# Performance work log

Measured on AMD Instinct MI355X. Metric: run time of the kernel, lower is better.

The kernel has to match this reference:

```python
import jax, jax.numpy as jnp
import numpy as np

C = 32
C_Z = 128
S = 256
N_SEQ = 256
LN_EPS = 1e-5


def setup_inputs() -> dict:
    key = jax.random.key(0)
    k1, k2, k3, k4 = jax.random.split(key, 4)
    m_si = jax.random.normal(k1, (S, N_SEQ, C), dtype=jnp.float32)
    ln_gamma = jnp.ones((C,), dtype=jnp.float32)
    ln_beta = jnp.zeros((C,), dtype=jnp.float32)
    # nn.Linear(c, 2c, bias=False): weight shape (2c, c)
    W_ab = jax.random.normal(k2, (2 * C, C), dtype=jnp.float32) / np.sqrt(C)
    # nn.Linear(c*c, c_z): weight (c_z, c*c), bias (c_z,)
    W_out = jax.random.normal(k3, (C_Z, C * C), dtype=jnp.float32) / np.sqrt(C * C)
    b_out = jax.random.normal(k4, (C_Z,), dtype=jnp.float32) * 0.01
    return {"m_si": m_si, "ln_gamma": ln_gamma, "ln_beta": ln_beta,
            "W_ab": W_ab, "W_out": W_out, "b_out": b_out}


def reference(m_si, ln_gamma, ln_beta, W_ab, W_out, b_out):
    # LayerNorm over channel dim c
    mu = jnp.mean(m_si, axis=-1, keepdims=True)
    var = jnp.var(m_si, axis=-1, keepdims=True)
    x = (m_si - mu) * jax.lax.rsqrt(var + LN_EPS) * ln_gamma + ln_beta
    # linear_no_bias then chunk into a, b: each (s, n_seq, c)
    ab = jnp.einsum('snc,dc->snd', x, W_ab)
    a, b = ab[..., :C], ab[..., C:]
    # mean over MSA sequences of outer products a[s,i,:] x b[s,j,:]
    # restructured as a contraction over n_seq: (i, j, c, c)
    outer = jnp.einsum('inc,jnd->ijcd', a, b) / N_SEQ
    outer = outer.reshape(S, S, C * C)  # flatten (c, c) -> c*c
    # final linear projection to c_z
    z_ij = jnp.einsum('ijk,zk->ijz', outer, W_out) + b_out
    return z_ij
```

## Files before the change

### kernel.cpp

```cpp
#include <hip/hip_runtime.h>

#define SDIM 256
#define NSEQ 256
#define CDIM 32
#define CZ 128
#define IB 8
#define JB 4

typedef __bf16 bfx8 __attribute__((ext_vector_type(8)));
typedef float fx4 __attribute__((ext_vector_type(4)));
typedef float f32x16 __attribute__((ext_vector_type(16)));
typedef unsigned int u32x4 __attribute__((ext_vector_type(4)));

__device__ __forceinline__ unsigned short f2bf(float f) {
  unsigned int u = __float_as_uint(f);
  u += 0x7fffu + ((u >> 16) & 1u);
  return (unsigned short)(u >> 16);
}

__device__ __forceinline__ unsigned int cvtpk(float lo, float hi) {
  unsigned int r;
  asm("v_cvt_pk_bf16_f32 %0, %1, %2" : "=v"(r) : "v"(lo), "v"(hi));
  return r;
}

__device__ __forceinline__ void gload16(const void* g, void* l) {
  __builtin_amdgcn_global_load_lds((const __attribute__((address_space(1))) unsigned int*)g,
                                   (__attribute__((address_space(3))) unsigned int*)l,
                                   16, 0, 0);
}


__global__ __launch_bounds__(256) void opm_prep(
    const float* __restrict__ m_si, const float* __restrict__ gamma, const float* __restrict__ beta,
    const float* __restrict__ Wab, const float* __restrict__ Wout,
    unsigned short* __restrict__ a_t, unsigned short* __restrict__ b_t,
    unsigned short* __restrict__ w2T)
{
  const int b = blockIdx.x;
  const int t = threadIdx.x;
  if (b < 2 * SDIM) {
    const int s = b >> 1, dph = b & 1;
    __shared__ float wab[1024];
    __shared__ float gbuf[64];
    __shared__ __align__(16) char xbuf[36864];
    float* xin = (float*)xbuf;
    unsigned short* xt = (unsigned short*)xbuf;

    const float* msrc = m_si + s * 8192;
#pragma unroll
    for (int k = 0; k < 8; ++k) {
      const int q = t + k * 256;
      const int row = q >> 3, cq = q & 7;
      ((fx4*)xin)[row * 9 + cq] = ((const fx4*)msrc)[q];
    }
    for (int k = t; k < 1024; k += 256) wab[k] = Wab[dph * 1024 + k];
    if (t < 32) { gbuf[t] = gamma[t]; gbuf[32 + t] = beta[t]; }
    __syncthreads();

    float x[CDIM];
#pragma unroll
    for (int c = 0; c < CDIM; ++c) x[c] = xin[t * 36 + c];
    __syncthreads();

    float mu = 0.f;
#pragma unroll
    for (int c = 0; c < CDIM; ++c) mu += x[c];
    mu *= (1.f / CDIM);
    float var = 0.f;
#pragma unroll
    for (int c = 0; c < CDIM; ++c) { float d = x[c] - mu; var += d * d; }
    var *= (1.f / CDIM);
    const float inv = rsqrtf(var + 1e-5f);
#pragma unroll
    for (int c = 0; c < CDIM; ++c) x[c] = (x[c] - mu) * inv * gbuf[c] + gbuf[32 + c];

    for (int dp = 0; dp < 32; ++dp) {
      float sum = 0.f;
#pragma unroll
      for (int c = 0; c < CDIM; ++c) sum += x[c] * wab[dp * 32 + c];
      xt[dp * 256 + t] = f2bf(sum);
    }
    __syncthreads();

    unsigned short* outb = dph ? b_t : a_t;
#pragma unroll
    for (int k = 0; k < 4; ++k) {
      const int q = t + k * 256;
      const int row = q >> 5, cc = q & 31;
      *(u32x4*)(outb + (s * 32 + row) * 256 + cc * 8) = *(const u32x4*)(xbuf + row * 512 + cc * 16);
    }
  } else {
    const int base = ((b - 2 * SDIM) * 256 + t) * 64;
#pragma unroll 8
    for (int u = 0; u < 64; ++u) {
      const int dest = base + u;
      const int e  = dest & 7;
      const int zl = (dest >> 3) & 31;
      const int h  = (dest >> 8) & 1;
      const int ks = (dest >> 9) & 63;
      const int zt = dest >> 15;
      const int kp = ks * 16 + h * 8 + e;
      const int c = (kp & 3) | (((kp >> 8) & 1) << 2) | (((kp >> 2) & 1) << 3) | (((kp >> 9) & 1) << 4);
      const int d = (kp >> 3) & 31;
      const int z = zt * 32 + zl;
      w2T[dest] = f2bf(Wout[z * 1024 + c * CDIM + d]);
    }
  }
}

__global__ __launch_bounds__(512, 4) void opm_main(
    const unsigned short* __restrict__ a_t, const unsigned short* __restrict__ b_t,
    const unsigned short* __restrict__ w2T, const float* __restrict__ bout,
    float* __restrict__ out)
{
  __shared__ __align__(16) char smem[65536];
  char* o_sh = smem;

  const int tid = threadIdx.x;
  const int lane = tid & 63;
  const int wid = tid >> 6;
  const int l31 = lane & 31;
  const int h = lane >> 5;

  const int bxr = blockIdx.x;
  const int bx = (bxr & 7) * 256 + (bxr >> 3);
  const int i0 = (bx >> 6) * IB;
  const int j0 = (bx & 63) * JB;

  const int wm = wid >> 1;
  const int wn = wid & 1;
  const int wbase = wid * 1024;

  f32x16 acc00 = {}, acc01 = {}, acc10 = {}, acc11 = {};

  auto STAGE = [&](int buf, int nc) {
    const int nbase = nc * 32;
    char* A = smem + 16384 + buf * 16384;
    char* B = smem + 49152 + buf * 8192;
#pragma unroll
    for (int pass = 0; pass < 2; ++pass) {
      const int q = pass * 512 + tid;
      const int row = q >> 2;
      const int gs = (q & 3) ^ ((q >> 3) & 3);
      const unsigned short* src = a_t + ((i0 + (row >> 5)) * 32 + (row & 31)) * 256 + nbase + gs * 8;
      gload16(src, A + pass * 8192 + wbase);
    }
    {
      const int q = tid;
      const int row = q >> 2;
      const int gs = (q & 3) ^ ((q >> 3) & 3);
      const unsigned short* src = b_t + ((j0 + (row >> 5)) * 32 + (row & 31)) * 256 + nbase + gs * 8;
      gload16(src, B + wbase);
    }
  };

  auto COMPUTE = [&](int buf) {
    char* A = smem + 16384 + buf * 16384;
    char* B = smem + 49152 + buf * 8192;
#pragma unroll
    for (int ks = 0; ks < 2; ++ks) {
      const int s = ks * 2 + h;
      bfx8 af0, af1, bf0, bf1;
      { const int r = wm * 64 + l31;      af0 = *(const bfx8*)(A + r * 64 + (((s ^ (r >> 1)) & 3) << 4)); }
      { const int r = wm * 64 + 32 + l31; af1 = *(const bfx8*)(A + r * 64 + (((s ^ (r >> 1)) & 3) << 4)); }
      { const int r = wn * 64 + l31;      bf0 = *(const bfx8*)(B + r * 64 + (((s ^ (r >> 1)) & 3) << 4)); }
      { const int r = wn * 64 + 32 + l31; bf1 = *(const bfx8*)(B + r * 64 + (((s ^ (r >> 1)) & 3) << 4)); }
      __builtin_amdgcn_s_setprio(1);
      acc00 = __builtin_amdgcn_mfma_f32_32x32x16_bf16(af0, bf0, acc00, 0, 0, 0);
      acc01 = __builtin_amdgcn_mfma_f32_32x32x16_bf16(af0, bf1, acc01, 0, 0, 0);
      acc10 = __builtin_amdgcn_mfma_f32_32x32x16_bf16(af1, bf0, acc10, 0, 0, 0);
      acc11 = __builtin_amdgcn_mfma_f32_32x32x16_bf16(af1, bf1, acc11, 0, 0, 0);
      __builtin_amdgcn_s_setprio(0);
    }
  };

  STAGE(0, 0);
#pragma unroll 2
  for (int t = 0; t < 8; ++t) {
    if (t < 7) {
      STAGE((t + 1) & 1, t + 1);
      asm volatile("s_waitcnt vmcnt(3)" ::: "memory");
    } else {
      asm volatile("s_waitcnt vmcnt(0)" ::: "memory");
    }
    __builtin_amdgcn_s_barrier();
    asm volatile("" ::: "memory");
    COMPUTE(t & 1);
    asm volatile("s_waitcnt lgkmcnt(0)" ::: "memory");
    __builtin_amdgcn_s_barrier();
  }

  {
    const f32x16 av[4] = { acc00 * 0.00390625f, acc01 * 0.00390625f,
                           acc10 * 0.00390625f, acc11 * 0.00390625f };
#pragma unroll
    for (int mi = 0; mi < 2; ++mi) {
#pragma unroll
      for (int ni = 0; ni < 2; ++ni) {
        const f32x16 a = av[mi * 2 + ni];
        const int p = (wm * 2 + mi) * 4 + (wn * 2 + ni);
#pragma unroll
        for (int c4 = 0; c4 < 2; ++c4) {
          const int sl = l31 + 32 * h + 64 * c4;
          u32x4 v;
          v[0] = cvtpk(a[8 * c4 + 0], a[8 * c4 + 1]);
          v[1] = cvtpk(a[8 * c4 + 2], a[8 * c4 + 3]);
          v[2] = cvtpk(a[8 * c4 + 4], a[8 * c4 + 5]);
          v[3] = cvtpk(a[8 * c4 + 6], a[8 * c4 + 7]);
          *(u32x4*)(o_sh + p * 2048 + ((sl ^ (p & 7)) << 4)) = v;
        }
      }
    }
  }
  __syncthreads();

  {
    const int zt = wid & 3;
    const int kh = wid >> 2;
    const unsigned short* wp = w2T + (zt << 15) + (h << 8) + (l31 << 3);
    f32x16 accB = {};
    int ksg = kh * 32;
    bfx8 wfA = *(const bfx8*)(wp + (ksg << 9));
    bfx8 ofA = *(const bfx8*)(o_sh + l31 * 2048 + (((2 * ksg + h) ^ (l31 & 7)) << 4));
#pragma unroll
    for (int it = 0; it < 31; ++it) {
      const int kn = kh * 32 + it + 1;
      const bfx8 wfB = *(const bfx8*)(wp + (kn << 9));
      const bfx8 ofB = *(const bfx8*)(o_sh + l31 * 2048 + (((2 * kn + h) ^ (l31 & 7)) << 4));
      accB = __builtin_amdgcn_mfma_f32_32x32x16_bf16(wfA, ofA, accB, 0, 0, 0);
      wfA = wfB; ofA = ofB;
    }
    accB = __builtin_amdgcn_mfma_f32_32x32x16_bf16(wfA, ofA, accB, 0, 0, 0);
    __syncthreads();

#pragma unroll
    for (int g2 = 0; g2 < 4; ++g2) {
      fx4 v = { accB[4 * g2], accB[4 * g2 + 1], accB[4 * g2 + 2], accB[4 * g2 + 3] };
      const int s = g2 * 2 + h;
      *(fx4*)(o_sh + kh * 16384 + zt * 4096 + ((s * 32 + l31) << 4)) = v;
    }
  }
  __syncthreads();

#pragma unroll
  for (int k = 0; k < 2; ++k) {
    const int v = tid + k * 512;
    const int zt2 = v >> 8, s2 = (v >> 5) & 7, pp = v & 31;
    const int off = zt2 * 4096 + ((s2 * 32 + pp) << 4);
    fx4 r = *(fx4*)(o_sh + off) + *(fx4*)(o_sh + 16384 + off);
    const int z0 = zt2 * 32 + s2 * 4;
    r += *(const fx4*)(bout + z0);
    const int i = i0 + (pp >> 2), j = j0 + (pp & 3);
    *(fx4*)(out + (i * SDIM + j) * CZ + z0) = r;
  }
}

extern "C" void kernel_launch(void* const* d_in, const int* in_sizes, int n_in,
                              void* d_out, int out_size, void* d_ws, size_t ws_size,
                              hipStream_t stream) {
  const float* m_si  = (const float*)d_in[0];
  const float* gamma = (const float*)d_in[1];
  const float* beta  = (const float*)d_in[2];
  const float* Wab   = (const float*)d_in[3];
  const float* Wout  = (const float*)d_in[4];
  const float* bout  = (const float*)d_in[5];
  float* out = (float*)d_out;

  char* ws = (char*)d_ws;
  unsigned short* a_t = (unsigned short*)ws;
  unsigned short* b_t = (unsigned short*)(ws + (4u << 20));
  unsigned short* w2T = (unsigned short*)(ws + (8u << 20));

  opm_prep<<<dim3(2 * SDIM + 8), dim3(256), 0, stream>>>(m_si, gamma, beta, Wab, Wout, a_t, b_t, w2T);
  opm_main<<<dim3(2048), dim3(512), 0, stream>>>(a_t, b_t, w2T, bout, out);
}
```

Before: 87.25 us.

## Deepen W prefetch in projection loop, vectorize prep, stage Wout transpose via LDS

In the main kernel's final projection, global weight fragments are now prefetched four steps ahead and LDS fragments two steps ahead, and s_setprio is raised around each MFMA. The goal is to hide global load latency behind the matrix ops. The output store becomes nontemporal to keep the write-once result from polluting the cache. In the prep kernel, the LayerNorm/linear dot product is vectorized with float4, and the Wout transpose-to-bf16 now loads Wout coalesced into shared memory before gathering, with 16-byte writes replacing scattered 2-byte global stores.

```diff
diff --git a/kernel.cpp b/kernel.cpp
--- a/kernel.cpp
+++ b/kernel.cpp
@@ -37,24 +37,23 @@
     unsigned short* __restrict__ a_t, unsigned short* __restrict__ b_t,
     unsigned short* __restrict__ w2T)
 {
+  __shared__ __align__(16) char shbuf[41216];
   const int b = blockIdx.x;
   const int t = threadIdx.x;
   if (b < 2 * SDIM) {
+    float* xin = (float*)shbuf;
+    unsigned short* xt = (unsigned short*)shbuf;
+    fx4* wab4 = (fx4*)(shbuf + 36864);
+    float* gbuf = (float*)(shbuf + 36864 + 4096);
     const int s = b >> 1, dph = b & 1;
-    __shared__ float wab[1024];
-    __shared__ float gbuf[64];
-    __shared__ __align__(16) char xbuf[36864];
-    float* xin = (float*)xbuf;
-    unsigned short* xt = (unsigned short*)xbuf;
 
     const float* msrc = m_si + s * 8192;
 #pragma unroll
     for (int k = 0; k < 8; ++k) {
       const int q = t + k * 256;
-      const int row = q >> 3, cq = q & 7;
-      ((fx4*)xin)[row * 9 + cq] = ((const fx4*)msrc)[q];
-    }
-    for (int k = t; k < 1024; k += 256) wab[k] = Wab[dph * 1024 + k];
+      ((fx4*)xin)[(q >> 3) * 9 + (q & 7)] = ((const fx4*)msrc)[q];
+    }
+    wab4[t & 255] = ((const fx4*)(Wab + dph * 1024))[t & 255];
     if (t < 32) { gbuf[t] = gamma[t]; gbuf[32 + t] = beta[t]; }
     __syncthreads();
 
@@ -72,14 +71,23 @@
     for (int c = 0; c < CDIM; ++c) { float d = x[c] - mu; var += d * d; }
     var *= (1.f / CDIM);
     const float inv = rsqrtf(var + 1e-5f);
-#pragma unroll
-    for (int c = 0; c < CDIM; ++c) x[c] = (x[c] - mu) * inv * gbuf[c] + gbuf[32 + c];
+    fx4 xv[8];
+#pragma unroll
+    for (int cq = 0; cq < 8; ++cq) {
+      fx4 v;
+#pragma unroll
+      for (int j = 0; j < 4; ++j) {
+        const int c = cq * 4 + j;
+        v[j] = (x[c] - mu) * inv * gbuf[c] + gbuf[32 + c];
+      }
+      xv[cq] = v;
+    }
 
     for (int dp = 0; dp < 32; ++dp) {
-      float sum = 0.f;
-#pragma unroll
-      for (int c = 0; c < CDIM; ++c) sum += x[c] * wab[dp * 32 + c];
-      xt[dp * 256 + t] = f2bf(sum);
+      fx4 a = xv[0] * wab4[dp * 8];
+#pragma unroll
+      for (int cq = 1; cq < 8; ++cq) a += xv[cq] * wab4[dp * 8 + cq];
+      xt[dp * 256 + t] = f2bf(a[0] + a[1] + a[2] + a[3]);
     }
     __syncthreads();
 
@@ -88,23 +96,38 @@
     for (int k = 0; k < 4; ++k) {
       const int q = t + k * 256;
       const int row = q >> 5, cc = q & 31;
-      *(u32x4*)(outb + (s * 32 + row) * 256 + cc * 8) = *(const u32x4*)(xbuf + row * 512 + cc * 16);
+      *(u32x4*)(outb + (s * 32 + row) * 256 + cc * 8) = *(const u32x4*)(shbuf + row * 512 + cc * 16);
     }
   } else {
-    const int base = ((b - 2 * SDIM) * 256 + t) * 64;
-#pragma unroll 8
-    for (int u = 0; u < 64; ++u) {
-      const int dest = base + u;
-      const int e  = dest & 7;
-      const int zl = (dest >> 3) & 31;
-      const int h  = (dest >> 8) & 1;
-      const int ks = (dest >> 9) & 63;
-      const int zt = dest >> 15;
-      const int kp = ks * 16 + h * 8 + e;
-      const int c = (kp & 3) | (((kp >> 8) & 1) << 2) | (((kp >> 2) & 1) << 3) | (((kp >> 9) & 1) << 4);
-      const int d = (kp >> 3) & 31;
-      const int z = zt * 32 + zl;
-      w2T[dest] = f2bf(Wout[z * 1024 + c * CDIM + d]);
+    unsigned short* lin = (unsigned short*)shbuf;
+    const int blk = b - 2 * SDIM;
+    const float* wsrc = Wout + blk * 16384;
+#pragma unroll
+    for (int jj = 0; jj < 16; ++jj) {
+      const int q = t + jj * 256;
+      const fx4 v = ((const fx4*)wsrc)[q];
+      unsigned short* dst = lin + q * 4;
+      dst[0] = f2bf(v[0]); dst[1] = f2bf(v[1]); dst[2] = f2bf(v[2]); dst[3] = f2bf(v[3]);
+    }
+    __syncthreads();
+    const int zt = blk >> 1;
+    const int zlbase = (blk & 1) * 16;
+#pragma unroll
+    for (int w = 0; w < 8; ++w) {
+      const int id = t + w * 256;
+      const int zll = id & 15;
+      const int h  = (id >> 4) & 1;
+      const int ks = id >> 5;
+      unsigned short vals[8];
+#pragma unroll
+      for (int e = 0; e < 8; ++e) {
+        const int kp = ks * 16 + h * 8 + e;
+        const int c = (kp & 3) | (((kp >> 8) & 1) << 2) | (((kp >> 2) & 1) << 3) | (((kp >> 9) & 1) << 4);
+        const int d = (kp >> 3) & 31;
+        vals[e] = lin[zll * 1024 + c * CDIM + d];
+      }
+      const int dest = (zt << 15) + (ks << 9) + (h << 8) + ((zlbase + zll) << 3);
+      *(u32x4*)(w2T + dest) = *(const u32x4*)vals;
     }
   }
 }
@@ -219,19 +242,28 @@
     const int zt = wid & 3;
     const int kh = wid >> 2;
     const unsigned short* wp = w2T + (zt << 15) + (h << 8) + (l31 << 3);
+    const int obase = l31 * 2048;
+    const int oxor = (l31 & 7) << 4;
+    bfx8 wfv[4], ofv[2];
+#pragma unroll
+    for (int pf = 0; pf < 4; ++pf) wfv[pf] = *(const bfx8*)(wp + ((kh * 32 + pf) << 9));
+#pragma unroll
+    for (int pf = 0; pf < 2; ++pf) {
+      const int sl = 2 * (kh * 32 + pf) + h;
+      ofv[pf] = *(const bfx8*)(o_sh + obase + ((sl << 4) ^ oxor));
+    }
     f32x16 accB = {};
-    int ksg = kh * 32;
-    bfx8 wfA = *(const bfx8*)(wp + (ksg << 9));
-    bfx8 ofA = *(const bfx8*)(o_sh + l31 * 2048 + (((2 * ksg + h) ^ (l31 & 7)) << 4));
-#pragma unroll
-    for (int it = 0; it < 31; ++it) {
-      const int kn = kh * 32 + it + 1;
-      const bfx8 wfB = *(const bfx8*)(wp + (kn << 9));
-      const bfx8 ofB = *(const bfx8*)(o_sh + l31 * 2048 + (((2 * kn + h) ^ (l31 & 7)) << 4));
-      accB = __builtin_amdgcn_mfma_f32_32x32x16_bf16(wfA, ofA, accB, 0, 0, 0);
-      wfA = wfB; ofA = ofB;
-    }
-    accB = __builtin_amdgcn_mfma_f32_32x32x16_bf16(wfA, ofA, accB, 0, 0, 0);
+#pragma unroll
+    for (int k = 0; k < 32; ++k) {
+      __builtin_amdgcn_s_setprio(1);
+      accB = __builtin_amdgcn_mfma_f32_32x32x16_bf16(wfv[k & 3], ofv[k & 1], accB, 0, 0, 0);
+      __builtin_amdgcn_s_setprio(0);
+      if (k + 4 < 32) wfv[k & 3] = *(const bfx8*)(wp + ((kh * 32 + k + 4) << 9));
+      if (k + 2 < 32) {
+        const int sl = 2 * (kh * 32 + k + 2) + h;
+        ofv[k & 1] = *(const bfx8*)(o_sh + obase + ((sl << 4) ^ oxor));
+      }
+    }
     __syncthreads();
 
 #pragma unroll
@@ -252,7 +284,7 @@
     const int z0 = zt2 * 32 + s2 * 4;
     r += *(const fx4*)(bout + z0);
     const int i = i0 + (pp >> 2), j = j0 + (pp & 3);
-    *(fx4*)(out + (i * SDIM + j) * CZ + z0) = r;
+    __builtin_nontemporal_store(r, (fx4*)(out + (i * SDIM + j) * CZ + z0));
   }
 }
 
```

After: 85.85 us. Within noise of the previous version (-1.6%).
